# Kernel tuning notes

Hardware: AMD Instinct MI355X
Metric: run time of the kernel (lower is better)

The kernel has to match this reference:

```python
import jax, jax.numpy as jnp
import numpy as np


def setup_inputs() -> dict:
    key = jax.random.key(0)
    ks = jax.random.split(key, 8)
    B, S, D, H = 32, 8192, 256, 256  # batch, seq_len, input_dim, hidden_dim
    bound = 1.0 / np.sqrt(H)
    x = jax.random.normal(ks[0], (B, H), dtype=jnp.float32)
    context = jax.random.normal(ks[1], (B, S, D), dtype=jnp.float32)
    mask = jax.random.randint(ks[2], (B, S), 0, 2, dtype=jnp.int32)
    # input_linear: Linear(H, H)
    W_in = jax.random.uniform(ks[3], (H, H), jnp.float32, -bound, bound)
    b_in = jax.random.uniform(ks[4], (H,), jnp.float32, -bound, bound)
    # context_linear: Conv1d(D, H, kernel=1) == pointwise linear over features
    W_ctx = jax.random.uniform(ks[5], (H, D), jnp.float32, -1.0 / np.sqrt(D), 1.0 / np.sqrt(D))
    b_ctx = jax.random.uniform(ks[6], (H,), jnp.float32, -1.0 / np.sqrt(D), 1.0 / np.sqrt(D))
    V = jax.random.uniform(ks[7], (H,), jnp.float32, -bound, bound)
    return {"x": x, "context": context, "mask": mask,
            "W_in": W_in, "b_in": b_in, "W_ctx": W_ctx, "b_ctx": b_ctx, "V": V}


def reference(x, context, mask, W_in, b_in, W_ctx, b_ctx, V):
    # inp: [B, H] -> broadcast over seq as [B, 1, H]
    inp = (x @ W_in.T + b_in)[:, None, :]
    # ctx: Conv1d(kernel=1) over permuted context == per-position linear: [B, S, H]
    ctx = jnp.einsum('bsd,hd->bsh', context, W_ctx) + b_ctx
    # score: V . tanh(inp + ctx) reduced over H -> [B, S]
    att = jnp.einsum('bsh,h->bs', jnp.tanh(inp + ctx), V)
    att = 10.0 * jnp.tanh(att)
    att = jnp.where(mask.astype(bool), att, -jnp.inf)
    ans = jax.nn.softmax(att, axis=1)
    indices = jnp.argmax(ans, axis=1)
    p = jnp.max(ans, axis=1)
    return (indices, p[:, None], mask.astype(bool))
```

## Files before the change

kernel.cpp:

```cpp
#include <hip/hip_runtime.h>
#include <math.h>

#define S_LEN 8192
#define BATCH 32
#define HDIM 256
#define DDIM 256
#define SCHUNK 1024
#define NSUB 16
#define TSUB 64
#define LDK 264

typedef float f32x4 __attribute__((ext_vector_type(4)));
typedef __fp16 h16x2 __attribute__((ext_vector_type(2)));
typedef __fp16 h16x4 __attribute__((ext_vector_type(4)));
typedef _Float16 f16x8 __attribute__((ext_vector_type(8)));

static __device__ __forceinline__ float fast_tanh(float x) {
    float e = __expf(2.0f * x);
    return 1.0f - 2.0f / (e + 1.0f);
}

static __device__ __forceinline__ void cvt_store(f32x4 v, _Float16* ph, _Float16* pl) {
    h16x2 h0 = __builtin_amdgcn_cvt_pkrtz(v[0], v[1]);
    h16x2 h1 = __builtin_amdgcn_cvt_pkrtz(v[2], v[3]);
    h16x2 l0 = __builtin_amdgcn_cvt_pkrtz(v[0] - (float)h0[0], v[1] - (float)h0[1]);
    h16x2 l1 = __builtin_amdgcn_cvt_pkrtz(v[2] - (float)h1[0], v[3] - (float)h1[1]);
    h16x4 hi; hi[0] = h0[0]; hi[1] = h0[1]; hi[2] = h1[0]; hi[3] = h1[1];
    h16x4 lo; lo[0] = l0[0]; lo[1] = l0[1]; lo[2] = l1[0]; lo[3] = l1[1];
    *(h16x4*)ph = hi;
    *(h16x4*)pl = lo;
}

__global__ void prep_kernel(const float* __restrict__ x,
                            const float* __restrict__ W_in,
                            const float* __restrict__ b_in,
                            const float* __restrict__ W_ctx,
                            const float* __restrict__ b_ctx,
                            float* __restrict__ cin,
                            _Float16* __restrict__ Wf) {
    __shared__ float xs[DDIM];
    const int bx = blockIdx.x;
    const int t  = threadIdx.x;
    if (bx < BATCH) {
        xs[t] = x[bx * DDIM + t];
        __syncthreads();
        const float* wr = W_in + t * DDIM;
        float acc = b_in[t] + b_ctx[t];
        #pragma unroll 8
        for (int d = 0; d < DDIM; ++d) acc += xs[d] * wr[d];
        cin[bx * HDIM + t] = acc;
    } else {
        const int g  = (bx - BATCH) * 256 + t;
        const int ht = g >> 9;
        const int ks = (g >> 6) & 7;
        const int l  = g & 63;
        const int h  = ht * 16 + (l & 15);
        const int d0 = ks * 32 + (l >> 4) * 8;
        const float* src = W_ctx + h * DDIM + d0;
        f16x8 vh;
        #pragma unroll
        for (int j = 0; j < 8; ++j) vh[j] = (_Float16)src[j];
        *(f16x8*)(Wf + (size_t)g * 8) = vh;
    }
}

__launch_bounds__(512, 2)
__global__ void att_kernel(const float* __restrict__ context,
                           const int* __restrict__ mask,
                           const float* __restrict__ cin,
                           const float* __restrict__ V,
                           const _Float16* __restrict__ Wf,
                           float* __restrict__ att,
                           float* __restrict__ out_mask) {
    __shared__ __align__(16) _Float16 a_hi[2][TSUB * LDK];
    __shared__ __align__(16) _Float16 a_lo[2][TSUB * LDK];
    __shared__ float att_part[2][8][TSUB];

    const int schunk = blockIdx.x;
    const int b      = blockIdx.y;
    const int t      = threadIdx.x;
    const int w      = t >> 6;
    const int l      = t & 63;
    const int lane16 = l & 15;
    const int q      = l >> 4;

    f16x8 wfrag[2][8];
    #pragma unroll
    for (int ht = 0; ht < 2; ++ht)
        #pragma unroll
        for (int ks = 0; ks < 8; ++ks)
            wfrag[ht][ks] = *(const f16x8*)(Wf + (size_t)(((w * 2 + ht) * 8 + ks) * 64 + l) * 8);

    f32x4 cinr4[2], vr4[2];
    #pragma unroll
    for (int ht = 0; ht < 2; ++ht)
        #pragma unroll
        for (int r = 0; r < 4; ++r) {
            int h = (w * 2 + ht) * 16 + q * 4 + r;
            cinr4[ht][r] = cin[b * HDIM + h];
            vr4[ht][r]   = V[h];
        }

    const float* cbase = context + ((size_t)b * S_LEN + (size_t)schunk * SCHUNK) * DDIM;

    #pragma unroll
    for (int i = 0; i < 8; ++i) {
        int f = i * 512 + t, row = f >> 6, c4 = f & 63;
        f32x4 v = *(const f32x4*)(cbase + row * DDIM + c4 * 4);
        cvt_store(v, &a_hi[0][row * LDK + c4 * 4], &a_lo[0][row * LDK + c4 * 4]);
    }
    __syncthreads();

    for (int it = 0; it < NSUB; ++it) {
        const int cur = it & 1;
        const bool pre = (it + 1 < NSUB);

        f32x4 pf[8];
        if (pre) {
            const float* nb = cbase + (size_t)(it + 1) * TSUB * DDIM;
            #pragma unroll
            for (int i = 0; i < 8; ++i) {
                int f = i * 512 + t, row = f >> 6, c4 = f & 63;
                pf[i] = *(const f32x4*)(nb + row * DDIM + c4 * 4);
            }
        }

        f32x4 acc[2][4];
        #pragma unroll
        for (int ht = 0; ht < 2; ++ht)
            #pragma unroll
            for (int nt = 0; nt < 4; ++nt) acc[ht][nt] = cinr4[ht];
        #pragma unroll
        for (int ks = 0; ks < 8; ++ks) {
            #pragma unroll
            for (int nt = 0; nt < 4; ++nt) {
                int o = (nt * 16 + lane16) * LDK + ks * 32 + q * 8;
                f16x8 bh = *(const f16x8*)(&a_hi[cur][o]);
                f16x8 bl = *(const f16x8*)(&a_lo[cur][o]);
                #pragma unroll
                for (int ht = 0; ht < 2; ++ht) {
                    acc[ht][nt] = __builtin_amdgcn_mfma_f32_16x16x32_f16(wfrag[ht][ks], bh, acc[ht][nt], 0, 0, 0);
                    acc[ht][nt] = __builtin_amdgcn_mfma_f32_16x16x32_f16(wfrag[ht][ks], bl, acc[ht][nt], 0, 0, 0);
                }
            }
        }

        #pragma unroll
        for (int nt = 0; nt < 4; ++nt) {
            float p = 0.f;
            #pragma unroll
            for (int ht = 0; ht < 2; ++ht)
                #pragma unroll
                for (int r = 0; r < 4; ++r)
                    p += fast_tanh(acc[ht][nt][r]) * vr4[ht][r];
            p += __shfl_xor(p, 16);
            p += __shfl_xor(p, 32);
            if (l < 16) att_part[cur][w][nt * 16 + l] = p;
        }

        if (pre) {
            #pragma unroll
            for (int i = 0; i < 8; ++i) {
                int f = i * 512 + t, row = f >> 6, c4 = f & 63;
                cvt_store(pf[i], &a_hi[cur ^ 1][row * LDK + c4 * 4],
                                 &a_lo[cur ^ 1][row * LDK + c4 * 4]);
            }
        }
        __syncthreads();

        if (t < TSUB) {
            float a = 0.f;
            #pragma unroll
            for (int ww = 0; ww < 8; ++ww) a += att_part[cur][ww][t];
            a = 10.0f * fast_tanh(a);
            int s  = schunk * SCHUNK + it * TSUB + t;
            int mk = mask[b * S_LEN + s];
            att[(size_t)b * S_LEN + s]      = mk ? a : -INFINITY;
            out_mask[(size_t)b * S_LEN + s] = mk ? 1.0f : 0.0f;
        }
    }
}

__global__ void reduce_kernel(const float* __restrict__ att,
                              float* __restrict__ out) {
    __shared__ float smax[1024];
    __shared__ int   sidx[1024];
    const int b = blockIdx.x;
    const int t = threadIdx.x;
    const float* row = att + (size_t)b * S_LEN;

    float best = -INFINITY;
    int   bid  = 0x7fffffff;
    for (int s = t; s < S_LEN; s += 1024) {
        float v = row[s];
        if (v > best) { best = v; bid = s; }
    }
    smax[t] = best; sidx[t] = bid;
    __syncthreads();
    for (int off = 512; off > 0; off >>= 1) {
        if (t < off) {
            float ov = smax[t + off]; int oi = sidx[t + off];
            if (ov > smax[t] || (ov == smax[t] && oi < sidx[t])) { smax[t] = ov; sidx[t] = oi; }
        }
        __syncthreads();
    }
    const float mx = smax[0];
    const int   ix = sidx[0];
    __syncthreads();

    float sum = 0.f;
    for (int s = t; s < S_LEN; s += 1024)
        sum += __expf(row[s] - mx);
    smax[t] = sum;
    __syncthreads();
    for (int off = 512; off > 0; off >>= 1) {
        if (t < off) smax[t] += smax[t + off];
        __syncthreads();
    }
    if (t == 0) {
        out[b]         = (float)ix;
        out[BATCH + b] = 1.0f / smax[0];
    }
}

extern "C" void kernel_launch(void* const* d_in, const int* in_sizes, int n_in,
                              void* d_out, int out_size, void* d_ws, size_t ws_size,
                              hipStream_t stream) {
    const float* x       = (const float*)d_in[0];
    const float* context = (const float*)d_in[1];
    const int*   mask    = (const int*)d_in[2];
    const float* W_in    = (const float*)d_in[3];
    const float* b_in    = (const float*)d_in[4];
    const float* W_ctx   = (const float*)d_in[5];
    const float* b_ctx   = (const float*)d_in[6];
    const float* V       = (const float*)d_in[7];
    float* out = (float*)d_out;

    char* ws = (char*)d_ws;
    float*    cin = (float*)ws;
    _Float16* Wf  = (_Float16*)(ws + 32 * 1024);
    float*    att = (float*)(ws + 160 * 1024);

    float* out_mask = out + 64;

    prep_kernel<<<64, 256, 0, stream>>>(x, W_in, b_in, W_ctx, b_ctx, cin, Wf);
    dim3 grid(S_LEN / SCHUNK, BATCH);
    att_kernel<<<grid, 512, 0, stream>>>(context, mask, cin, V, Wf, att, out_mask);
    reduce_kernel<<<BATCH, 1024, 0, stream>>>(att, out);
}
```

Baseline: 400.7 us.

## Fuse softmax max/argmax reduction into attention kernel via atomics

```diff
diff --git a/kernel.cpp b/kernel.cpp
--- a/kernel.cpp
+++ b/kernel.cpp
@@ -37,11 +37,19 @@
                             const float* __restrict__ W_ctx,
                             const float* __restrict__ b_ctx,
                             float* __restrict__ cin,
-                            _Float16* __restrict__ Wf) {
+                            _Float16* __restrict__ Wf,
+                            unsigned long long* __restrict__ pmax,
+                            float* __restrict__ psum,
+                            int* __restrict__ pcnt) {
     __shared__ float xs[DDIM];
     const int bx = blockIdx.x;
     const int t  = threadIdx.x;
     if (bx < BATCH) {
+        if (t == 0) {
+            pmax[bx] = 0ull;
+            psum[bx] = 0.0f;
+            pcnt[bx] = 0;
+        }
         xs[t] = x[bx * DDIM + t];
         __syncthreads();
         const float* wr = W_in + t * DDIM;
@@ -70,8 +78,11 @@
                            const float* __restrict__ cin,
                            const float* __restrict__ V,
                            const _Float16* __restrict__ Wf,
-                           float* __restrict__ att,
-                           float* __restrict__ out_mask) {
+                           float* __restrict__ out,
+                           float* __restrict__ out_mask,
+                           unsigned long long* __restrict__ pmax,
+                           float* __restrict__ psum,
+                           int* __restrict__ pcnt) {
     __shared__ __align__(16) _Float16 a_hi[2][TSUB * LDK];
     __shared__ __align__(16) _Float16 a_lo[2][TSUB * LDK];
     __shared__ float att_part[2][8][TSUB];
@@ -102,6 +113,10 @@
         }
 
     const float* cbase = context + ((size_t)b * S_LEN + (size_t)schunk * SCHUNK) * DDIM;
+
+    float best = -INFINITY;
+    int   bid  = 0x7fffffff;
+    float sume = 0.0f;
 
     #pragma unroll
     for (int i = 0; i < 8; ++i) {
@@ -175,51 +190,44 @@
             a = 10.0f * fast_tanh(a);
             int s  = schunk * SCHUNK + it * TSUB + t;
             int mk = mask[b * S_LEN + s];
-            att[(size_t)b * S_LEN + s]      = mk ? a : -INFINITY;
             out_mask[(size_t)b * S_LEN + s] = mk ? 1.0f : 0.0f;
-        }
-    }
-}
-
-__global__ void reduce_kernel(const float* __restrict__ att,
-                              float* __restrict__ out) {
-    __shared__ float smax[1024];
-    __shared__ int   sidx[1024];
-    const int b = blockIdx.x;
-    const int t = threadIdx.x;
-    const float* row = att + (size_t)b * S_LEN;
-
-    float best = -INFINITY;
-    int   bid  = 0x7fffffff;
-    for (int s = t; s < S_LEN; s += 1024) {
-        float v = row[s];
-        if (v > best) { best = v; bid = s; }
-    }
-    smax[t] = best; sidx[t] = bid;
-    __syncthreads();
-    for (int off = 512; off > 0; off >>= 1) {
-        if (t < off) {
-            float ov = smax[t + off]; int oi = sidx[t + off];
-            if (ov > smax[t] || (ov == smax[t] && oi < sidx[t])) { smax[t] = ov; sidx[t] = oi; }
-        }
-        __syncthreads();
-    }
-    const float mx = smax[0];
-    const int   ix = sidx[0];
-    __syncthreads();
-
-    float sum = 0.f;
-    for (int s = t; s < S_LEN; s += 1024)
-        sum += __expf(row[s] - mx);
-    smax[t] = sum;
-    __syncthreads();
-    for (int off = 512; off > 0; off >>= 1) {
-        if (t < off) smax[t] += smax[t + off];
-        __syncthreads();
-    }
-    if (t == 0) {
-        out[b]         = (float)ix;
-        out[BATCH + b] = 1.0f / smax[0];
+            if (mk) {
+                if (a > best) { best = a; bid = s; }
+                sume += __expf(a - 10.0f);
+            }
+        }
+    }
+
+    if (w == 0) {
+        #pragma unroll
+        for (int off = 32; off > 0; off >>= 1) {
+            float ov = __shfl_xor(best, off);
+            int   oi = __shfl_xor(bid, off);
+            float os = __shfl_xor(sume, off);
+            sume += os;
+            if (ov > best || (ov == best && oi < bid)) { best = ov; bid = oi; }
+        }
+        if (l == 0) {
+            unsigned ub = __float_as_uint(best);
+            ub = (ub & 0x80000000u) ? ~ub : (ub | 0x80000000u);
+            unsigned long long pk =
+                ((unsigned long long)ub << 32) | (unsigned long long)(0xFFFFFFFFu - (unsigned)bid);
+            atomicMax(&pmax[b], pk);
+            atomicAdd(&psum[b], sume);
+            __threadfence();
+            int old = atomicAdd(&pcnt[b], 1);
+            if (old == 7) {
+                __threadfence();
+                unsigned long long m = atomicMax(&pmax[b], 0ull);
+                float ssum = atomicAdd(&psum[b], 0.0f);
+                unsigned mb = (unsigned)(m >> 32);
+                float mv = (mb & 0x80000000u) ? __uint_as_float(mb ^ 0x80000000u)
+                                              : __uint_as_float(~mb);
+                int idx = (int)(0xFFFFFFFFu - (unsigned)(m & 0xFFFFFFFFull));
+                out[b]         = (float)idx;
+                out[BATCH + b] = __expf(mv - 10.0f) / ssum;
+            }
+        }
     }
 }
 
@@ -237,14 +245,17 @@
     float* out = (float*)d_out;
 
     char* ws = (char*)d_ws;
-    float*    cin = (float*)ws;
-    _Float16* Wf  = (_Float16*)(ws + 32 * 1024);
-    float*    att = (float*)(ws + 160 * 1024);
+    float*              cin  = (float*)ws;
+    _Float16*           Wf   = (_Float16*)(ws + 32 * 1024);
+    unsigned long long* pmax = (unsigned long long*)(ws + 160 * 1024);
+    float*              psum = (float*)(ws + 160 * 1024 + 256);
+    int*                pcnt = (int*)(ws + 160 * 1024 + 384);
 
     float* out_mask = out + 64;
 
-    prep_kernel<<<64, 256, 0, stream>>>(x, W_in, b_in, W_ctx, b_ctx, cin, Wf);
+    prep_kernel<<<64, 256, 0, stream>>>(x, W_in, b_in, W_ctx, b_ctx, cin, Wf,
+                                        pmax, psum, pcnt);
     dim3 grid(S_LEN / SCHUNK, BATCH);
-    att_kernel<<<grid, 512, 0, stream>>>(context, mask, cin, V, Wf, att, out_mask);
-    reduce_kernel<<<BATCH, 1024, 0, stream>>>(att, out);
-}
+    att_kernel<<<grid, 512, 0, stream>>>(context, mask, cin, V, Wf,
+                                         out, out_mask, pmax, psum, pcnt);
+}
```

Result: no change. 394.8 us (median of 2 runs) (-1.5%).
